# Optimization experiments

Hardware: AMD Instinct MI355X
Metric: run time of the kernel (lower is better)

## Reference

```python
import jax, jax.numpy as jnp
import numpy as np

N, E = 20000, 100000
F_IN, F_OUT = 1024, 512
NUM_FILT = 8
DIM = 3  # output_dim per coordinate-function type (4 types -> 12 total)


def _death_indices(f, edge_index):
    """0-dim persistence pairing via union-find over a vertex filtration.
    Returns death[v]: index of the node whose filtration value kills the
    component created by v (death[v] == v for unpaired/essential nodes)."""
    u, v = edge_index[0], edge_index[1]
    fu, fv = f[u], f[v]
    d_idx = jnp.where(fu >= fv, u, v)          # node realizing the edge value max(f[u], f[v])
    order = jnp.argsort(jnp.maximum(fu, fv))   # process edges in increasing filtration order
    edges = jnp.stack([u[order], v[order], d_idx[order]], axis=1)  # [E, 3]
    n = f.shape[0]

    def find(parent, i):
        return jax.lax.while_loop(lambda j: parent[j] != j, lambda j: parent[j], i)

    def step(carry, e):
        parent, death = carry
        ra = find(parent, e[0])
        rb = find(parent, e[1])
        older = jnp.where(f[ra] <= f[rb], ra, rb)   # older (smaller birth) component survives
        younger = ra + rb - older                   # the other root dies at this edge
        merge = ra != rb
        parent = jnp.where(merge, parent.at[younger].set(older), parent)
        death = jnp.where(merge, death.at[younger].set(e[2]), death)
        return (parent, death), None

    idx = jnp.arange(n)
    (_, death), _ = jax.lax.scan(step, (idx, idx), edges)
    return death


def _coord_activations(p, tri_t, gauss_mu, gauss_sigma, line_w, rhat_c, rhat_r):
    """p: [N, 2] persistence pairs -> [N, 4*DIM] coordinate-function features."""
    b, d = p[:, 0:1], p[:, 1:2]
    tri = jax.nn.relu(d - jnp.abs(tri_t[None, :] - b))                     # Triangle_transform
    diff = p[:, None, :] - gauss_mu[None, :, :]
    gauss = jnp.exp(-jnp.sum(diff * diff, -1) / (2.0 * gauss_sigma ** 2))  # Gaussian_transform
    line = p @ line_w.T                                                    # Line_transform
    q = jnp.sum(jnp.abs(p[:, None, :] - rhat_c[None, :, :]), -1)
    rhat = 1.0 / (1.0 + q) - 1.0 / (1.0 + jnp.abs(jnp.abs(rhat_r) - q))    # RationalHat_transform
    return jnp.concatenate([tri, gauss, line, rhat], axis=1)


def _forward(x, filt_w, filt_b, tri_t, gauss_mu, gauss_sigma, line_w,
             rhat_c, rhat_r, out_w, out_b, edge_index):
    f_all = (x @ filt_w.T + filt_b).T                     # [NUM_FILT, N] filtration values
    f_sg = jax.lax.stop_gradient(f_all)                   # pairing structure is combinatorial
    death = jax.vmap(lambda ff: _death_indices(ff, edge_index))(f_sg)  # [NUM_FILT, N] int
    pairs = jnp.stack([f_all, jnp.take_along_axis(f_all, death, axis=1)], axis=-1)  # [F, N, 2]
    acts = jax.vmap(lambda p: _coord_activations(p, tri_t, gauss_mu, gauss_sigma,
                                                 line_w, rhat_c, rhat_r))(pairs)  # [F, N, 12]
    coord = jnp.transpose(acts, (1, 0, 2)).reshape(x.shape[0], -1)  # torch.cat over filtrations
    return jnp.concatenate([x, coord], axis=1) @ out_w.T + out_b


def setup_inputs() -> dict:
    key = jax.random.key(0)
    ks = jax.random.split(key, 10)
    s = 0.02
    return {
        "x": jax.random.normal(ks[0], (N, F_IN), jnp.float32),
        "edge_index": jax.random.randint(ks[1], (2, E), 0, N),
        "filt_w": jax.random.normal(ks[2], (NUM_FILT, F_IN), jnp.float32) * s,
        "filt_b": jnp.zeros((NUM_FILT,), jnp.float32),
        "tri_t": jax.random.normal(ks[3], (DIM,), jnp.float32),
        "gauss_mu": jax.random.normal(ks[4], (DIM, 2), jnp.float32),
        "gauss_sigma": jnp.asarray(0.5, jnp.float32),
        "line_w": jax.random.normal(ks[5], (DIM, 2), jnp.float32),
        "rhat_c": jax.random.normal(ks[6], (DIM, 2), jnp.float32),
        "rhat_r": jnp.asarray(1.0, jnp.float32),
        "out_w": jax.random.normal(ks[7], (F_OUT, F_IN + NUM_FILT * 4 * DIM), jnp.float32) * s,
        "out_b": jnp.zeros((F_OUT,), jnp.float32),
    }


def reference(x, edge_index, filt_w, filt_b, tri_t, gauss_mu, gauss_sigma,
              line_w, rhat_c, rhat_r, out_w, out_b):
    return _forward(x, filt_w, filt_b, tri_t, gauss_mu, gauss_sigma,
                    line_w, rhat_c, rhat_r, out_w, out_b, edge_index)
```

## Files before the change

kernel.cpp:

```cpp
#include <hip/hip_runtime.h>
#include <stdint.h>

#define NV 20000
#define NE 100000
#define NK 8
#define FIN 1024
#define FOUT 512
#define FTOT 1120
#define KP 1152
#define MP 20096
#define CAP 4096
#define ROUNDS 13
#define NB 32
#define CHUNK (NE / NB)
#define LDA 72

typedef unsigned int u32;
typedef unsigned long long u64;
typedef unsigned short u16;
typedef __attribute__((ext_vector_type(8))) short bf16x8;
typedef __attribute__((ext_vector_type(4))) float f32x4;

__device__ __forceinline__ u32 sb(float x) {
    u32 u = __float_as_uint(x);
    return u ^ ((u & 0x80000000u) ? 0xFFFFFFFFu : 0x80000000u);
}
__device__ __forceinline__ float isb(u32 s) {
    u32 u = (s & 0x80000000u) ? (s ^ 0x80000000u) : ~s;
    return __uint_as_float(u);
}
__device__ __forceinline__ u16 f2bf(float f) {
    u32 u = __float_as_uint(f);
    return (u16)((u + 0x7FFFu + ((u >> 16) & 1u)) >> 16);
}

__global__ __launch_bounds__(256) void k_fx(
    const float* __restrict__ x, const float* __restrict__ fw,
    const float* __restrict__ fb, float* __restrict__ f, u16* __restrict__ A) {
    __shared__ float w[NK * FIN];
    __shared__ float xs[4][FIN];
    for (int i = threadIdx.x; i < NK * FIN; i += 256) w[i] = fw[i];
    __syncthreads();
    int wave = threadIdx.x >> 6, lane = threadIdx.x & 63;
    int v = blockIdx.x * 4 + wave;
    float4* xd = (float4*)xs[wave];
    if (v < NV) {
        const float4* xr4 = (const float4*)(x + (size_t)v * FIN);
        for (int i = lane; i < FIN / 4; i += 64) xd[i] = xr4[i];
    } else {
        for (int i = lane; i < FIN / 4; i += 64) xd[i] = make_float4(0.f, 0.f, 0.f, 0.f);
    }
    float acc[NK];
#pragma unroll
    for (int k = 0; k < NK; k++) acc[k] = 0.f;
    for (int c = 0; c < FIN / 64; c++) {
        int i = c * 64 + lane;
        float xv = xs[wave][i];
#pragma unroll
        for (int k = 0; k < NK; k++) acc[k] = fmaf(xv, w[k * FIN + i], acc[k]);
    }
#pragma unroll
    for (int off = 32; off >= 1; off >>= 1)
#pragma unroll
        for (int k = 0; k < NK; k++) acc[k] += __shfl_xor(acc[k], off, 64);
    if (v < NV && lane < NK) f[lane * NV + v] = acc[lane] + fb[lane];
    for (int cc = lane; cc < 144; cc += 64) {
        int c0 = cc * 8;
        u32 pk[4];
        if (c0 < FIN) {
#pragma unroll
            for (int j = 0; j < 4; j++)
                pk[j] = (u32)f2bf(xs[wave][c0 + 2 * j]) |
                        ((u32)f2bf(xs[wave][c0 + 2 * j + 1]) << 16);
        } else {
#pragma unroll
            for (int j = 0; j < 4; j++) pk[j] = 0u;
        }
        *(uint4*)(A + (size_t)v * KP + c0) = make_uint4(pk[0], pk[1], pk[2], pk[3]);
    }
}

__global__ void k_init(u32* __restrict__ comp, u64* __restrict__ cand, u32* cnts) {
    int t = blockIdx.x * 256 + threadIdx.x;
    comp[t] = (u32)(t % CAP);
    cand[t] = ~0ull;
    if (t < 32) cnts[t] = 0;
}

__global__ void k_castw(const float* __restrict__ ow, u16* __restrict__ W) {
    int t = blockIdx.x * 256 + threadIdx.x;
    if (t >= FOUT * 144) return;
    int n = t / 144, c = (t % 144) * 8;
    u32 pk[4];
    if (c < FTOT) {
        const float* wr = ow + (size_t)n * FTOT + c;
#pragma unroll
        for (int j = 0; j < 4; j++)
            pk[j] = (u32)f2bf(wr[2 * j]) | ((u32)f2bf(wr[2 * j + 1]) << 16);
    } else {
#pragma unroll
        for (int j = 0; j < 4; j++) pk[j] = 0u;
    }
    *(uint4*)(W + (size_t)n * KP + c) = make_uint4(pk[0], pk[1], pk[2], pk[3]);
}

__global__ void k_initdesc(const float* __restrict__ f, u64* __restrict__ cd,
                           float* __restrict__ dval) {
    int t = blockIdx.x * 256 + threadIdx.x;
    u32 v = (u32)(t % NV);
    float fv = f[t];
    cd[t] = ((u64)sb(fv) << 32) | v;
    dval[t] = fv;
}

__global__ void k_descedge(const int* __restrict__ ei, const float* __restrict__ f,
                           u64* __restrict__ cd) {
    int t = blockIdx.x * 256 + threadIdx.x;
    int k = t / NE, e = t % NE;
    int a = ei[e], b = ei[NE + e];
    if (a == b) return;
    float fa = f[k * NV + a], fb2 = f[k * NV + b];
    int d, l; float fl;
    if (fa >= fb2) { d = a; l = b; fl = fb2; } else { d = b; l = a; fl = fa; }
    u64 key = ((u64)sb(fl) << 32) | (u32)l;
    atomicMin(&cd[k * NV + d], key);
}

__global__ __launch_bounds__(1024) void k_basmin(
    const u64* __restrict__ cd, u32* __restrict__ db,
    u32* nmin, u32* __restrict__ mlist) {
    __shared__ u32 nxt[NV];
    __shared__ u16 dsh[NV];
    __shared__ u32 changed;
    int k = blockIdx.x;
    const u64* c = cd + (size_t)k * NV;
    for (int i = threadIdx.x; i < NV; i += 1024) nxt[i] = (u32)c[i];
    if (threadIdx.x == 0) changed = 0u;
    __syncthreads();
    for (int pass = 0; pass < 16; pass++) {
        bool ch = false;
        for (int i = threadIdx.x; i < NV; i += 1024) {
            u32 a = nxt[i];
            u32 b = nxt[a];
            if (b != a) {
                u32 c2 = nxt[b];
                u32 d2 = nxt[c2];
                nxt[i] = d2;
                ch = true;
            }
        }
        if (ch) changed = 1u;
        __syncthreads();
        u32 done = (changed == 0u);
        __syncthreads();
        if (threadIdx.x == 0) changed = 0u;
        __syncthreads();
        if (done) break;
    }
    for (int i = threadIdx.x; i < NV; i += 1024) {
        if (nxt[i] == (u32)i) {
            u32 id = atomicAdd(&nmin[k], 1u);
            if (id < CAP) { mlist[k * CAP + id] = (u32)i; dsh[i] = (u16)id; }
        }
    }
    __syncthreads();
    for (int i = threadIdx.x; i < NV; i += 1024)
        db[k * NV + i] = (u32)dsh[nxt[i]];
}

__global__ void k_edgeprep(const int* __restrict__ ei, const float* __restrict__ f,
                           const u32* __restrict__ db,
                           u64* __restrict__ wkey, u32* __restrict__ ep) {
    int t = blockIdx.x * 256 + threadIdx.x;
    int k = t / NE, e = t % NE;
    int a = ei[e], b = ei[NE + e];
    if (a == b) { ep[t] = 0xFFFFFFFFu; return; }
    float fa = f[k * NV + a], fb2 = f[k * NV + b];
    float w = (fa >= fb2) ? fa : fb2;
    wkey[t] = ((u64)sb(w) << 32) | (u32)e;
    u32 da = db[k * NV + a], db2 = db[k * NV + b];
    if (da == db2) { ep[t] = 0xFFFFFFFFu; return; }
    ep[t] = (da << 16) | db2;
}

__device__ __forceinline__ u32 rootofs(const u32* c, u32 i) {
    while (true) { u32 p = c[i]; if (p == i) return i; i = p; }
}

__global__ void k_candA(u32* __restrict__ ep, const u64* __restrict__ wkey,
                        const u32* __restrict__ comp_g, u64* __restrict__ cand_g,
                        const u32* __restrict__ done) {
    __shared__ u32 scomp[CAP];
    __shared__ u64 scand[CAP];
    int k = blockIdx.y, b = blockIdx.x;
    if (done[k]) return;
    for (int i = threadIdx.x; i < CAP; i += 256) {
        scomp[i] = comp_g[k * CAP + i];
        scand[i] = ~0ull;
    }
    __syncthreads();
    int e0 = b * CHUNK;
    u32* epk = ep + (size_t)k * NE;
    const u64* wkk = wkey + (size_t)k * NE;
    for (int e = e0 + threadIdx.x; e < e0 + CHUNK; e += 256) {
        u32 p32 = epk[e];
        if (p32 & 0x80000000u) continue;
        u32 A = rootofs(scomp, p32 >> 16), B = rootofs(scomp, p32 & 0xFFFFu);
        if (A == B) { epk[e] = p32 | 0x80000000u; continue; }
        u64 w = wkk[e];
        atomicMin(&scand[A], w);
        atomicMin(&scand[B], w);
    }
    __syncthreads();
    u64* cnd = cand_g + (size_t)k * CAP;
    for (int i = threadIdx.x; i < CAP; i += 256) {
        u64 v = scand[i];
        if (v != ~0ull) atomicMin(&cnd[i], v);
    }
}

__global__ void k_round(u64* __restrict__ cand_g, const u32* __restrict__ ep,
                        u32* __restrict__ comp_g, u32* mstcnt,
                        u64* __restrict__ mkey, u32* __restrict__ done) {
    __shared__ u64 scand[CAP];
    __shared__ u32 scomp[CAP];
    __shared__ u32 shk[CAP];
    __shared__ u32 nmerge;
    int k = blockIdx.x;
    if (done[k]) return;
    if (threadIdx.x == 0) nmerge = 0;
    for (int i = threadIdx.x; i < CAP; i += 1024) {
        scand[i] = cand_g[k * CAP + i];
        scomp[i] = comp_g[k * CAP + i];
    }
    __syncthreads();
    for (int i = threadIdx.x; i < CAP; i += 1024) {
        u64 cc = scand[i];
        if (cc == ~0ull) { shk[i] = (u32)i; continue; }
        u32 e = (u32)cc;
        u32 p32 = ep[(size_t)k * NE + e];
        u32 A = rootofs(scomp, p32 >> 16), B = rootofs(scomp, p32 & 0xFFFFu);
        shk[i] = (A == (u32)i) ? B : A;
    }
    __syncthreads();
    for (int i = threadIdx.x; i < CAP; i += 1024) {
        u32 o = shk[i];
        if (o == (u32)i) continue;
        bool mutual = (shk[o] == (u32)i);
        if (mutual && (u32)i < o) continue;
        scomp[i] = o;
        u64 cc = scand[i];
        u32 j = atomicAdd(&mstcnt[k], 1u);
        atomicAdd(&nmerge, 1u);
        if (j < CAP) mkey[k * CAP + j] = cc;
    }
    __syncthreads();
    for (int i = threadIdx.x; i < CAP; i += 1024) scomp[i] = rootofs(scomp, i);
    __syncthreads();
    for (int i = threadIdx.x; i < CAP; i += 1024) {
        comp_g[k * CAP + i] = scomp[i];
        cand_g[k * CAP + i] = ~0ull;
    }
    if (threadIdx.x == 0 && nmerge == 0) done[k] = 1;
}

__global__ __launch_bounds__(1024) void k_sort(const u32* mstcnt, u64* __restrict__ mkey) {
    __shared__ u64 skey[CAP];
    int k = blockIdx.x;
    u32 cnt = mstcnt[k]; if (cnt > CAP) cnt = CAP;
    int n2 = 64; while (n2 < (int)cnt) n2 <<= 1;
    for (int i = threadIdx.x; i < n2; i += 1024)
        skey[i] = (i < (int)cnt) ? mkey[k * CAP + i] : ~0ull;
    __syncthreads();
    int half = n2 >> 1;
    for (int sz = 2; sz <= n2; sz <<= 1) {
        for (int st = sz >> 1; st >= 1; st >>= 1) {
            for (int t = threadIdx.x; t < half; t += 1024) {
                int i = ((t & ~(st - 1)) << 1) | (t & (st - 1));
                int j = i | st;
                bool up = ((i & sz) == 0);
                u64 a = skey[i], b = skey[j];
                if (up ? (a > b) : (a < b)) { skey[i] = b; skey[j] = a; }
            }
            __syncthreads();
        }
    }
    for (int i = threadIdx.x; i < (int)cnt; i += 1024)
        mkey[k * CAP + i] = skey[i];
}

__global__ __launch_bounds__(64) void k_pairw(
    const u32* nmin, const u32* __restrict__ mlist, const u32* mstcnt,
    const u64* __restrict__ mkey, const u32* __restrict__ ep,
    const float* __restrict__ f, float* __restrict__ dval) {
    __shared__ u32 par[CAP];
    __shared__ u32 val[CAP];
    __shared__ u32 tag[CAP];
    int k = blockIdx.x;
    int lane = threadIdx.x;
    u32 nm = nmin[k]; if (nm > CAP) nm = CAP;
    u32 cnt = mstcnt[k]; if (cnt > CAP) cnt = CAP;
    for (int i = lane; i < CAP; i += 64) {
        par[i] = (u32)i;
        tag[i] = 0u;
        val[i] = (i < (int)nm) ? __float_as_uint(f[k * NV + mlist[k * CAP + i]]) : 0u;
    }
    __syncthreads();
    u32 nw = (cnt + 63) >> 6;
    u64 nkey = 0; u32 npay = 0;
    if ((u32)lane < cnt) {
        nkey = mkey[(size_t)k * CAP + lane];
        npay = ep[(size_t)k * NE + (u32)nkey] & 0x7FFFFFFFu;
    }
    for (u32 w = 0; w < nw; w++) {
        u64 key = nkey; u32 pay = npay;
        bool valid = (w * 64 + (u32)lane) < cnt;
        u32 jn = (w + 1) * 64 + (u32)lane;
        if (jn < cnt) {
            nkey = mkey[(size_t)k * CAP + jn];
            npay = ep[(size_t)k * NE + (u32)nkey] & 0x7FFFFFFFu;
        }
        u32 wb = (u32)(key >> 32);
        u32 la = pay >> 16, lb = pay & 0xFFFFu;
        u32 rA = la, rB = lb;
        if (valid) {
            while (true) {
                u32 pA = par[rA], pB = par[rB];
                bool dA = (pA == rA), dB = (pB == rB);
                if (dA && dB) break;
                if (!dA) { u32 g = par[pA]; par[rA] = g; rA = g; }
                if (!dB) { u32 g = par[pB]; par[rB] = g; rB = g; }
            }
        }
        u32 vA = valid ? val[rA] : 0u;
        u32 vB = valid ? val[rB] : 0u;
        if (valid) { atomicAdd(&tag[rA], 1u); atomicAdd(&tag[rB], 1u); }
        u32 cA = rA, cvA = vA, cB = rB, cvB = vB;
        u32 t_fy = 0xFFFFFFFFu, t_fo = 0u, t_fvo = 0u;
        if (valid) {
            if (__uint_as_float(cvA) <= __uint_as_float(cvB)) { t_fo = cA; t_fvo = cvA; t_fy = cB; }
            else                                              { t_fo = cB; t_fvo = cvB; t_fy = cA; }
        }
        u32 pkd = (t_fy << 16) | (t_fo & 0xFFFFu);
        bool pend = valid && (atomicAdd(&tag[t_fy], 0u) > 1u);
        u64 m = __ballot(pend);
        while (m) {
            u32 s = (u32)__builtin_ctzll(m);
            m &= m - 1;
            u32 opk = __builtin_amdgcn_readlane(pkd, (int)s);
            u32 ov  = __builtin_amdgcn_readlane(t_fvo, (int)s);
            u32 oy = opk >> 16, oo = opk & 0xFFFFu;
            if ((u32)lane == s) pend = false;
            bool app = valid && ((u32)lane > s);
            bool mA = app && (cA == oy);
            bool mB = app && (cB == oy);
            if (mA) { cA = oo; cvA = ov; }
            if (mB) { cB = oo; cvB = ov; }
            bool rm = mA || mB;
            if (__any(rm)) {
                if (rm) {
                    atomicAdd(&tag[oo], 1u);
                    if (__uint_as_float(cvA) <= __uint_as_float(cvB)) { t_fo = cA; t_fvo = cvA; t_fy = cB; }
                    else                                              { t_fo = cB; t_fvo = cvB; t_fy = cA; }
                    pkd = (t_fy << 16) | (t_fo & 0xFFFFu);
                    pend = atomicAdd(&tag[t_fy], 0u) > 1u;
                }
                m = __ballot(pend);
                m &= (s < 63u) ? (~0ull << (s + 1)) : 0ull;
            }
        }
        if (valid) { tag[rA] = 0u; tag[rB] = 0u; }
        if (valid) { par[t_fy] = t_fo; val[t_fy] = wb; }
        __syncthreads();
    }
    for (int i = lane; i < (int)nm; i += 64) {
        if (par[i] != (u32)i)
            dval[k * NV + mlist[k * CAP + i]] = isb(val[i]);
    }
}

__global__ void k_coordb(const float* __restrict__ f, const float* __restrict__ dval,
                         const float* __restrict__ tri_t, const float* __restrict__ gmu,
                         const float* __restrict__ gsig, const float* __restrict__ lw,
                         const float* __restrict__ rc, const float* __restrict__ rr,
                         u16* __restrict__ A) {
    int t = blockIdx.x * 256 + threadIdx.x;
    int k = t / NV, v = t % NV;
    float b = f[t], d = dval[t];
    float o[12];
    float s = gsig[0];
    float inv2s2 = 1.0f / (2.0f * s * s);
    float r = fabsf(rr[0]);
#pragma unroll
    for (int j = 0; j < 3; j++) {
        float tri = d - fabsf(tri_t[j] - b);
        o[j] = tri > 0.f ? tri : 0.f;
        float dx = b - gmu[2 * j], dy = d - gmu[2 * j + 1];
        o[3 + j] = expf(-(dx * dx + dy * dy) * inv2s2);
        o[6 + j] = b * lw[2 * j] + d * lw[2 * j + 1];
        float q = fabsf(b - rc[2 * j]) + fabsf(d - rc[2 * j + 1]);
        o[9 + j] = 1.0f / (1.0f + q) - 1.0f / (1.0f + fabsf(r - q));
    }
    u16* dst = A + (size_t)v * KP + FIN + k * 12;
    u32* d32 = (u32*)dst;
#pragma unroll
    for (int j = 0; j < 6; j++)
        d32[j] = (u32)f2bf(o[2 * j]) | ((u32)f2bf(o[2 * j + 1]) << 16);
}

__global__ __launch_bounds__(512, 2) void k_gemm2(
    const u16* __restrict__ A, const u16* __restrict__ W,
    const float* __restrict__ bias, float* __restrict__ out) {
    __shared__ u16 As[128 * LDA];
    __shared__ u16 Ws[512 * LDA];
    int m0 = blockIdx.x * 128;
    int t = threadIdx.x;
    int wave = t >> 6, lane = t & 63;
    int wr = wave >> 2, wc = wave & 3;
    int lrow = lane & 15, lq = lane >> 4;
    f32x4 acc[4][8];
#pragma unroll
    for (int mt = 0; mt < 4; mt++)
#pragma unroll
        for (int nt = 0; nt < 8; nt++) acc[mt][nt] = (f32x4){0.f, 0.f, 0.f, 0.f};

    int arow[2], acol[2], wrow[8], wcol[8];
    uint4 av[2], wv[8];
#pragma unroll
    for (int i = 0; i < 2; i++) {
        int c = i * 512 + t;
        arow[i] = c >> 3; acol[i] = (c & 7) * 8;
        av[i] = *(const uint4*)(A + (size_t)(m0 + arow[i]) * KP + acol[i]);
    }
#pragma unroll
    for (int i = 0; i < 8; i++) {
        int c = i * 512 + t;
        wrow[i] = c >> 3; wcol[i] = (c & 7) * 8;
        wv[i] = *(const uint4*)(W + (size_t)wrow[i] * KP + wcol[i]);
    }
#pragma unroll 1
    for (int step = 0; step < KP / 64; step++) {
        __syncthreads();
#pragma unroll
        for (int i = 0; i < 2; i++) *(uint4*)(As + arow[i] * LDA + acol[i]) = av[i];
#pragma unroll
        for (int i = 0; i < 8; i++) *(uint4*)(Ws + wrow[i] * LDA + wcol[i]) = wv[i];
        __syncthreads();
        int k0n = (step + 1 < KP / 64) ? (step + 1) * 64 : 0;
#pragma unroll
        for (int i = 0; i < 2; i++)
            av[i] = *(const uint4*)(A + (size_t)(m0 + arow[i]) * KP + k0n + acol[i]);
#pragma unroll
        for (int i = 0; i < 8; i++)
            wv[i] = *(const uint4*)(W + (size_t)wrow[i] * KP + k0n + wcol[i]);
#pragma unroll
        for (int kh = 0; kh < 2; kh++) {
            int kk = kh * 32 + lq * 8;
            bf16x8 af[4], wf[8];
#pragma unroll
            for (int mt = 0; mt < 4; mt++)
                af[mt] = *(const bf16x8*)(As + (wr * 64 + mt * 16 + lrow) * LDA + kk);
#pragma unroll
            for (int nt = 0; nt < 8; nt++)
                wf[nt] = *(const bf16x8*)(Ws + (wc * 128 + nt * 16 + lrow) * LDA + kk);
#pragma unroll
            for (int mt = 0; mt < 4; mt++)
#pragma unroll
                for (int nt = 0; nt < 8; nt++)
                    acc[mt][nt] = __builtin_amdgcn_mfma_f32_16x16x32_bf16(
                        af[mt], wf[nt], acc[mt][nt], 0, 0, 0);
        }
    }
    __syncthreads();
    float* scr = (float*)Ws + wave * 576;
    int cg = lane & 7;
    int rr8 = lane >> 3;
#pragma unroll
    for (int np = 0; np < 4; np++) {
        int o = wc * 128 + np * 32 + cg * 4;
        f32x4 b4 = *(const f32x4*)(bias + o);
#pragma unroll
        for (int mt = 0; mt < 4; mt++) {
#pragma unroll
            for (int fh = 0; fh < 2; fh++) {
                f32x4 fr = acc[mt][2 * np + fh];
#pragma unroll
                for (int i = 0; i < 4; i++)
                    scr[(lq * 4 + i) * 36 + fh * 16 + lrow] = fr[i];
            }
#pragma unroll
            for (int p = 0; p < 2; p++) {
                int r = p * 8 + rr8;
                f32x4 vv = *(f32x4*)(scr + r * 36 + cg * 4);
                int v = m0 + wr * 64 + mt * 16 + r;
                if (v < NV) *(f32x4*)(out + (size_t)v * FOUT + o) = vv + b4;
            }
        }
    }
}

extern "C" void kernel_launch(void* const* d_in, const int* in_sizes, int n_in,
                              void* d_out, int out_size, void* d_ws, size_t ws_size,
                              hipStream_t stream) {
    const float* x     = (const float*)d_in[0];
    const int*   ei    = (const int*)d_in[1];
    const float* fw    = (const float*)d_in[2];
    const float* fbv   = (const float*)d_in[3];
    const float* tri_t = (const float*)d_in[4];
    const float* gmu   = (const float*)d_in[5];
    const float* gsig  = (const float*)d_in[6];
    const float* lw    = (const float*)d_in[7];
    const float* rc    = (const float*)d_in[8];
    const float* rr    = (const float*)d_in[9];
    const float* ow    = (const float*)d_in[10];
    const float* ob    = (const float*)d_in[11];
    float* out = (float*)d_out;

    char* p = (char*)d_ws;
    auto alloc = [&](size_t bytes) -> void* {
        void* q = (void*)p;
        p += (bytes + 255) & ~(size_t)255;
        return q;
    };
    float* f     = (float*)alloc((size_t)NK * NV * 4);
    u64*   cd    = (u64*)  alloc((size_t)NK * NV * 8);
    u32*   db    = (u32*)  alloc((size_t)NK * NV * 4);
    u32*   mlist = (u32*)  alloc((size_t)NK * CAP * 4);
    u32*   cnts  = (u32*)  alloc(64 * 4);
    u64*   wkey  = (u64*)  alloc((size_t)NK * NE * 8);
    u32*   ep    = (u32*)  alloc((size_t)NK * NE * 4);
    u32*   comp  = (u32*)  alloc((size_t)NK * CAP * 4);
    u64*   cand  = (u64*)  alloc((size_t)NK * CAP * 8);
    u64*   mkey  = (u64*)  alloc((size_t)NK * CAP * 8);
    float* dval  = (float*)alloc((size_t)NK * NV * 4);
    u16*   Ab    = (u16*)  alloc((size_t)MP * KP * 2);
    u16*   Wb    = (u16*)  alloc((size_t)FOUT * KP * 2);
    u32* nmin = cnts; u32* mstcnt = cnts + 8; u32* done = cnts + 16;

    k_init<<<128, 256, 0, stream>>>(comp, cand, cnts);
    k_fx<<<MP / 4, 256, 0, stream>>>(x, fw, fbv, f, Ab);
    k_castw<<<(FOUT * 144 + 255) / 256, 256, 0, stream>>>(ow, Wb);
    k_initdesc<<<625, 256, 0, stream>>>(f, cd, dval);
    k_descedge<<<3125, 256, 0, stream>>>(ei, f, cd);
    k_basmin<<<NK, 1024, 0, stream>>>(cd, db, nmin, mlist);
    k_edgeprep<<<3125, 256, 0, stream>>>(ei, f, db, wkey, ep);
    for (int r = 0; r < ROUNDS; r++) {
        k_candA<<<dim3(NB, NK), 256, 0, stream>>>(ep, wkey, comp, cand, done);
        k_round<<<NK, 1024, 0, stream>>>(cand, ep, comp, mstcnt, mkey, done);
    }
    k_sort<<<8, 1024, 0, stream>>>(mstcnt, mkey);
    k_pairw<<<8, 64, 0, stream>>>(nmin, mlist, mstcnt, mkey, ep, f, dval);
    k_coordb<<<625, 256, 0, stream>>>(f, dval, tri_t, gmu, gsig, lw, rc, rr, Ab);
    k_gemm2<<<157, 512, 0, stream>>>(Ab, Wb, ob, out);
}
```

Before: 667.7 us.

## Fuse Boruvka rounds and sort into one persistent per-filtration kernel

Replaces the 13-round loop of k_candA/k_round launches plus the separate sort with a single k_msf kernel. It runs one 1024-thread block per filtration, keeps the component and candidate arrays in LDS for the whole run, and exits early once a round finds no merge. It also skips atomicMin calls when the candidate is already smaller, and folds the counter reset into k_initdesc. The intent is to remove about 27 launches and the global round-trips of comp/cand state. In exchange, only 8 blocks scan all 100k edges each round, where before 32 blocks per filtration shared that scan, so the available parallelism drops.

```diff
diff --git a/kernel.cpp b/kernel.cpp
--- a/kernel.cpp
+++ b/kernel.cpp
@@ -11,8 +11,6 @@
 #define MP 20096
 #define CAP 4096
 #define ROUNDS 13
-#define NB 32
-#define CHUNK (NE / NB)
 #define LDA 72
 
 typedef unsigned int u32;
@@ -80,13 +78,6 @@
     }
 }
 
-__global__ void k_init(u32* __restrict__ comp, u64* __restrict__ cand, u32* cnts) {
-    int t = blockIdx.x * 256 + threadIdx.x;
-    comp[t] = (u32)(t % CAP);
-    cand[t] = ~0ull;
-    if (t < 32) cnts[t] = 0;
-}
-
 __global__ void k_castw(const float* __restrict__ ow, u16* __restrict__ W) {
     int t = blockIdx.x * 256 + threadIdx.x;
     if (t >= FOUT * 144) return;
@@ -105,12 +96,13 @@
 }
 
 __global__ void k_initdesc(const float* __restrict__ f, u64* __restrict__ cd,
-                           float* __restrict__ dval) {
+                           float* __restrict__ dval, u32* __restrict__ cnts) {
     int t = blockIdx.x * 256 + threadIdx.x;
     u32 v = (u32)(t % NV);
     float fv = f[t];
     cd[t] = ((u64)sb(fv) << 32) | v;
     dval[t] = fv;
+    if (t < 64) cnts[t] = 0;
 }
 
 __global__ void k_descedge(const int* __restrict__ ei, const float* __restrict__ f,
@@ -187,106 +179,83 @@
     while (true) { u32 p = c[i]; if (p == i) return i; i = p; }
 }
 
-__global__ void k_candA(u32* __restrict__ ep, const u64* __restrict__ wkey,
-                        const u32* __restrict__ comp_g, u64* __restrict__ cand_g,
-                        const u32* __restrict__ done) {
+__global__ __launch_bounds__(1024) void k_msf(
+    u32* __restrict__ ep, const u64* __restrict__ wkey,
+    u32* __restrict__ mstcnt, u64* __restrict__ mkey) {
     __shared__ u32 scomp[CAP];
     __shared__ u64 scand[CAP];
-    int k = blockIdx.y, b = blockIdx.x;
-    if (done[k]) return;
-    for (int i = threadIdx.x; i < CAP; i += 256) {
-        scomp[i] = comp_g[k * CAP + i];
-        scand[i] = ~0ull;
-    }
-    __syncthreads();
-    int e0 = b * CHUNK;
+    __shared__ u32 shk[CAP];
+    __shared__ u64 smkey[CAP];
+    __shared__ u32 nmerge, totm;
+    int k = blockIdx.x;
+    int tid = threadIdx.x;
     u32* epk = ep + (size_t)k * NE;
     const u64* wkk = wkey + (size_t)k * NE;
-    for (int e = e0 + threadIdx.x; e < e0 + CHUNK; e += 256) {
-        u32 p32 = epk[e];
-        if (p32 & 0x80000000u) continue;
-        u32 A = rootofs(scomp, p32 >> 16), B = rootofs(scomp, p32 & 0xFFFFu);
-        if (A == B) { epk[e] = p32 | 0x80000000u; continue; }
-        u64 w = wkk[e];
-        atomicMin(&scand[A], w);
-        atomicMin(&scand[B], w);
-    }
-    __syncthreads();
-    u64* cnd = cand_g + (size_t)k * CAP;
-    for (int i = threadIdx.x; i < CAP; i += 256) {
-        u64 v = scand[i];
-        if (v != ~0ull) atomicMin(&cnd[i], v);
-    }
-}
-
-__global__ void k_round(u64* __restrict__ cand_g, const u32* __restrict__ ep,
-                        u32* __restrict__ comp_g, u32* mstcnt,
-                        u64* __restrict__ mkey, u32* __restrict__ done) {
-    __shared__ u64 scand[CAP];
-    __shared__ u32 scomp[CAP];
-    __shared__ u32 shk[CAP];
-    __shared__ u32 nmerge;
-    int k = blockIdx.x;
-    if (done[k]) return;
-    if (threadIdx.x == 0) nmerge = 0;
-    for (int i = threadIdx.x; i < CAP; i += 1024) {
-        scand[i] = cand_g[k * CAP + i];
-        scomp[i] = comp_g[k * CAP + i];
-    }
-    __syncthreads();
-    for (int i = threadIdx.x; i < CAP; i += 1024) {
-        u64 cc = scand[i];
-        if (cc == ~0ull) { shk[i] = (u32)i; continue; }
-        u32 e = (u32)cc;
-        u32 p32 = ep[(size_t)k * NE + e];
-        u32 A = rootofs(scomp, p32 >> 16), B = rootofs(scomp, p32 & 0xFFFFu);
-        shk[i] = (A == (u32)i) ? B : A;
-    }
-    __syncthreads();
-    for (int i = threadIdx.x; i < CAP; i += 1024) {
-        u32 o = shk[i];
-        if (o == (u32)i) continue;
-        bool mutual = (shk[o] == (u32)i);
-        if (mutual && (u32)i < o) continue;
-        scomp[i] = o;
-        u64 cc = scand[i];
-        u32 j = atomicAdd(&mstcnt[k], 1u);
-        atomicAdd(&nmerge, 1u);
-        if (j < CAP) mkey[k * CAP + j] = cc;
-    }
-    __syncthreads();
-    for (int i = threadIdx.x; i < CAP; i += 1024) scomp[i] = rootofs(scomp, i);
-    __syncthreads();
-    for (int i = threadIdx.x; i < CAP; i += 1024) {
-        comp_g[k * CAP + i] = scomp[i];
-        cand_g[k * CAP + i] = ~0ull;
-    }
-    if (threadIdx.x == 0 && nmerge == 0) done[k] = 1;
-}
-
-__global__ __launch_bounds__(1024) void k_sort(const u32* mstcnt, u64* __restrict__ mkey) {
-    __shared__ u64 skey[CAP];
-    int k = blockIdx.x;
-    u32 cnt = mstcnt[k]; if (cnt > CAP) cnt = CAP;
+    for (int i = tid; i < CAP; i += 1024) { scomp[i] = (u32)i; scand[i] = ~0ull; }
+    if (tid == 0) totm = 0u;
+    __syncthreads();
+    for (int r = 0; r < ROUNDS; r++) {
+        if (tid == 0) nmerge = 0u;
+        for (int e = tid; e < NE; e += 1024) {
+            u32 p32 = epk[e];
+            if (p32 & 0x80000000u) continue;
+            u32 A = rootofs(scomp, p32 >> 16), B = rootofs(scomp, p32 & 0xFFFFu);
+            if (A == B) { epk[e] = p32 | 0x80000000u; continue; }
+            u64 w = wkk[e];
+            if (w < scand[A]) atomicMin(&scand[A], w);
+            if (w < scand[B]) atomicMin(&scand[B], w);
+        }
+        __syncthreads();
+        for (int i = tid; i < CAP; i += 1024) {
+            u64 cc = scand[i];
+            if (cc == ~0ull) { shk[i] = (u32)i; continue; }
+            u32 e = (u32)cc;
+            u32 p32 = epk[e] & 0x7FFFFFFFu;
+            u32 A = rootofs(scomp, p32 >> 16), B = rootofs(scomp, p32 & 0xFFFFu);
+            shk[i] = (A == (u32)i) ? B : A;
+        }
+        __syncthreads();
+        for (int i = tid; i < CAP; i += 1024) {
+            u32 o = shk[i];
+            if (o == (u32)i) continue;
+            bool mutual = (shk[o] == (u32)i);
+            if (mutual && (u32)i < o) continue;
+            scomp[i] = o;
+            u64 cc = scand[i];
+            u32 j = atomicAdd(&totm, 1u);
+            atomicAdd(&nmerge, 1u);
+            if (j < CAP) smkey[j] = cc;
+        }
+        __syncthreads();
+        for (int i = tid; i < CAP; i += 1024) scomp[i] = rootofs(scomp, i);
+        __syncthreads();
+        u32 nm = nmerge;
+        for (int i = tid; i < CAP; i += 1024) scand[i] = ~0ull;
+        __syncthreads();
+        if (nm == 0u) break;
+    }
+    u32 tm = totm;
+    if (tid == 0) mstcnt[k] = tm;
+    u32 cnt = tm; if (cnt > CAP) cnt = CAP;
     int n2 = 64; while (n2 < (int)cnt) n2 <<= 1;
-    for (int i = threadIdx.x; i < n2; i += 1024)
-        skey[i] = (i < (int)cnt) ? mkey[k * CAP + i] : ~0ull;
+    for (int i = tid; i < n2; i += 1024)
+        if (i >= (int)cnt) smkey[i] = ~0ull;
     __syncthreads();
     int half = n2 >> 1;
     for (int sz = 2; sz <= n2; sz <<= 1) {
         for (int st = sz >> 1; st >= 1; st >>= 1) {
-            for (int t = threadIdx.x; t < half; t += 1024) {
+            for (int t = tid; t < half; t += 1024) {
                 int i = ((t & ~(st - 1)) << 1) | (t & (st - 1));
                 int j = i | st;
                 bool up = ((i & sz) == 0);
-                u64 a = skey[i], b = skey[j];
-                if (up ? (a > b) : (a < b)) { skey[i] = b; skey[j] = a; }
+                u64 a = smkey[i], b = smkey[j];
+                if (up ? (a > b) : (a < b)) { smkey[i] = b; smkey[j] = a; }
             }
             __syncthreads();
         }
     }
-    for (int i = threadIdx.x; i < (int)cnt; i += 1024)
-        mkey[k * CAP + i] = skey[i];
+    for (int i = tid; i < (int)cnt; i += 1024)
+        mkey[(size_t)k * CAP + i] = smkey[i];
 }
 
 __global__ __launch_bounds__(64) void k_pairw(
@@ -529,26 +498,19 @@
     u32*   cnts  = (u32*)  alloc(64 * 4);
     u64*   wkey  = (u64*)  alloc((size_t)NK * NE * 8);
     u32*   ep    = (u32*)  alloc((size_t)NK * NE * 4);
-    u32*   comp  = (u32*)  alloc((size_t)NK * CAP * 4);
-    u64*   cand  = (u64*)  alloc((size_t)NK * CAP * 8);
     u64*   mkey  = (u64*)  alloc((size_t)NK * CAP * 8);
     float* dval  = (float*)alloc((size_t)NK * NV * 4);
     u16*   Ab    = (u16*)  alloc((size_t)MP * KP * 2);
     u16*   Wb    = (u16*)  alloc((size_t)FOUT * KP * 2);
-    u32* nmin = cnts; u32* mstcnt = cnts + 8; u32* done = cnts + 16;
-
-    k_init<<<128, 256, 0, stream>>>(comp, cand, cnts);
+    u32* nmin = cnts; u32* mstcnt = cnts + 8;
+
     k_fx<<<MP / 4, 256, 0, stream>>>(x, fw, fbv, f, Ab);
     k_castw<<<(FOUT * 144 + 255) / 256, 256, 0, stream>>>(ow, Wb);
-    k_initdesc<<<625, 256, 0, stream>>>(f, cd, dval);
+    k_initdesc<<<625, 256, 0, stream>>>(f, cd, dval, cnts);
     k_descedge<<<3125, 256, 0, stream>>>(ei, f, cd);
     k_basmin<<<NK, 1024, 0, stream>>>(cd, db, nmin, mlist);
     k_edgeprep<<<3125, 256, 0, stream>>>(ei, f, db, wkey, ep);
-    for (int r = 0; r < ROUNDS; r++) {
-        k_candA<<<dim3(NB, NK), 256, 0, stream>>>(ep, wkey, comp, cand, done);
-        k_round<<<NK, 1024, 0, stream>>>(cand, ep, comp, mstcnt, mkey, done);
-    }
-    k_sort<<<8, 1024, 0, stream>>>(mstcnt, mkey);
+    k_msf<<<NK, 1024, 0, stream>>>(ep, wkey, mstcnt, mkey);
     k_pairw<<<8, 64, 0, stream>>>(nmin, mlist, mstcnt, mkey, ep, f, dval);
     k_coordb<<<625, 256, 0, stream>>>(f, dval, tri_t, gmu, gsig, lw, rc, rr, Ab);
     k_gemm2<<<157, 512, 0, stream>>>(Ab, Wb, ob, out);
```

Measured after the change: 874.0 us. 30.9% more time.

## Load GEMM MFMA fragments directly from global memory instead of LDS staging

Applied to the files above, without the earlier changes.

The output GEMM kernel drops its shared-memory staging of A and W tiles and their double-buffered register prefetch. Each wave now reads its bf16 MFMA fragments straight from global memory, relying on L1/L2 for reuse, and the per-wave epilogue scratch gets its own small shared buffer. This removes the block barriers and LDS traffic in the K loop, but it gives up explicit cross-wave reuse and the prefetch overlap, so global and cache load traffic rises. It also masks the top bit of the packed edge-endpoint word in the MST merge kernel, and relaxes launch bounds.

```diff
diff --git a/kernel.cpp b/kernel.cpp
--- a/kernel.cpp
+++ b/kernel.cpp
@@ -238,7 +238,7 @@
         u64 cc = scand[i];
         if (cc == ~0ull) { shk[i] = (u32)i; continue; }
         u32 e = (u32)cc;
-        u32 p32 = ep[(size_t)k * NE + e];
+        u32 p32 = ep[(size_t)k * NE + e] & 0x7FFFFFFFu;
         u32 A = rootofs(scomp, p32 >> 16), B = rootofs(scomp, p32 & 0xFFFFu);
         shk[i] = (A == (u32)i) ? B : A;
     }
@@ -408,11 +408,10 @@
         d32[j] = (u32)f2bf(o[2 * j]) | ((u32)f2bf(o[2 * j + 1]) << 16);
 }
 
-__global__ __launch_bounds__(512, 2) void k_gemm2(
+__global__ __launch_bounds__(512) void k_gemm2(
     const u16* __restrict__ A, const u16* __restrict__ W,
     const float* __restrict__ bias, float* __restrict__ out) {
-    __shared__ u16 As[128 * LDA];
-    __shared__ u16 Ws[512 * LDA];
+    __shared__ float scr8[8 * 576];
     int m0 = blockIdx.x * 128;
     int t = threadIdx.x;
     int wave = t >> 6, lane = t & 63;
@@ -424,45 +423,28 @@
 #pragma unroll
         for (int nt = 0; nt < 8; nt++) acc[mt][nt] = (f32x4){0.f, 0.f, 0.f, 0.f};
 
-    int arow[2], acol[2], wrow[8], wcol[8];
-    uint4 av[2], wv[8];
-#pragma unroll
-    for (int i = 0; i < 2; i++) {
-        int c = i * 512 + t;
-        arow[i] = c >> 3; acol[i] = (c & 7) * 8;
-        av[i] = *(const uint4*)(A + (size_t)(m0 + arow[i]) * KP + acol[i]);
-    }
-#pragma unroll
-    for (int i = 0; i < 8; i++) {
-        int c = i * 512 + t;
-        wrow[i] = c >> 3; wcol[i] = (c & 7) * 8;
-        wv[i] = *(const uint4*)(W + (size_t)wrow[i] * KP + wcol[i]);
-    }
+    const u16* Ab[4];
+    const u16* Wb2[8];
+#pragma unroll
+    for (int mt = 0; mt < 4; mt++)
+        Ab[mt] = A + (size_t)(m0 + wr * 64 + mt * 16 + lrow) * KP + lq * 8;
+#pragma unroll
+    for (int nt = 0; nt < 8; nt++)
+        Wb2[nt] = W + (size_t)(wc * 128 + nt * 16 + lrow) * KP + lq * 8;
+
 #pragma unroll 1
     for (int step = 0; step < KP / 64; step++) {
-        __syncthreads();
-#pragma unroll
-        for (int i = 0; i < 2; i++) *(uint4*)(As + arow[i] * LDA + acol[i]) = av[i];
-#pragma unroll
-        for (int i = 0; i < 8; i++) *(uint4*)(Ws + wrow[i] * LDA + wcol[i]) = wv[i];
-        __syncthreads();
-        int k0n = (step + 1 < KP / 64) ? (step + 1) * 64 : 0;
-#pragma unroll
-        for (int i = 0; i < 2; i++)
-            av[i] = *(const uint4*)(A + (size_t)(m0 + arow[i]) * KP + k0n + acol[i]);
-#pragma unroll
-        for (int i = 0; i < 8; i++)
-            wv[i] = *(const uint4*)(W + (size_t)wrow[i] * KP + k0n + wcol[i]);
+        int kb = step * 64;
 #pragma unroll
         for (int kh = 0; kh < 2; kh++) {
-            int kk = kh * 32 + lq * 8;
+            int kk = kb + kh * 32;
             bf16x8 af[4], wf[8];
 #pragma unroll
             for (int mt = 0; mt < 4; mt++)
-                af[mt] = *(const bf16x8*)(As + (wr * 64 + mt * 16 + lrow) * LDA + kk);
+                af[mt] = *(const bf16x8*)(Ab[mt] + kk);
 #pragma unroll
             for (int nt = 0; nt < 8; nt++)
-                wf[nt] = *(const bf16x8*)(Ws + (wc * 128 + nt * 16 + lrow) * LDA + kk);
+                wf[nt] = *(const bf16x8*)(Wb2[nt] + kk);
 #pragma unroll
             for (int mt = 0; mt < 4; mt++)
 #pragma unroll
@@ -471,8 +453,7 @@
                         af[mt], wf[nt], acc[mt][nt], 0, 0, 0);
         }
     }
-    __syncthreads();
-    float* scr = (float*)Ws + wave * 576;
+    float* scr = scr8 + wave * 576;
     int cg = lane & 7;
     int rr8 = lane >> 3;
 #pragma unroll
```

Result: no change. 674.0 us (+0.9%).
